# Optimization experiments

Hardware: AMD Instinct MI355X
Metric: run time of the kernel (lower is better)

The kernel has to match this reference:

```python
import jax, jax.numpy as jnp
import numpy as np

M = 4096
N = 4096

def _twiddle(L):
    k = jnp.arange(L, dtype=jnp.float32)
    ang = -np.pi * k / (2.0 * L)
    return jnp.stack([jnp.cos(ang), jnp.sin(ang)], axis=-1).astype(jnp.float32)  # [L,2] = exp(-i*pi*k/(2L))

def setup_inputs() -> dict:
    key = jax.random.key(0)
    x = jax.random.normal(key, (M, N), dtype=jnp.float32)
    return {"x": x, "expkM": _twiddle(M), "expkN": _twiddle(N)}

def reference(x, expkM, expkN):
    # 2D DCT-II via Makhoul even/odd reordering + single complex FFT2 + twiddle multiply.
    # out[u,v] = sum_{m,n} x[m,n] cos(pi*u*(2m+1)/(2M)) cos(pi*v*(2n+1)/(2N))
    Mh, Nh = x.shape
    permM = jnp.concatenate([jnp.arange(0, Mh, 2), jnp.arange(Mh - 1, 0, -2)])
    permN = jnp.concatenate([jnp.arange(0, Nh, 2), jnp.arange(Nh - 1, 0, -2)])
    y = x[permM][:, permN]                       # even/odd reorder in both dims
    Y = jnp.fft.fft2(y)                          # [M,N] complex
    wM = expkM[:, 0] + 1j * expkM[:, 1]          # exp(-i*pi*u/(2M))
    wN = expkN[:, 0] + 1j * expkN[:, 1]          # exp(-i*pi*v/(2N))
    Yrev = jnp.roll(Y[::-1, :], 1, axis=0)       # Y[(M-u) % M, v]
    C = 0.5 * (wN[None, :] * Y + jnp.conj(wN)[None, :] * jnp.conj(Yrev))
    return jnp.real(wM[:, None] * C)
```

## Files before the change

kernel.cpp:

```cpp
#include <hip/hip_runtime.h>
#include <math.h>

#define NFULL 4096
#define NH    2048
#define T     256

__device__ __forceinline__ int pad(int i) { return i + (i >> 3); }

__device__ __forceinline__ float2 cmul(float2 a, float2 b) {
    return make_float2(a.x * b.x - a.y * b.y, a.x * b.y + a.y * b.x);
}

__device__ __forceinline__ float2 sc(float ang) {
    float s, c;
    __sincosf(ang, &s, &c);
    return make_float2(c, s);
}

__device__ __forceinline__ void dft8(float2 v[8]) {
    const float s = 0.70710678118654752f;
    float2 e0 = v[0], o0 = v[1], e1 = v[2], o1 = v[3];
    float2 e2 = v[4], o2 = v[5], e3 = v[6], o3 = v[7];
    float2 t0 = make_float2(e0.x + e2.x, e0.y + e2.y);
    float2 t1 = make_float2(e0.x - e2.x, e0.y - e2.y);
    float2 t2 = make_float2(e1.x + e3.x, e1.y + e3.y);
    float2 t3 = make_float2(e1.x - e3.x, e1.y - e3.y);
    float2 E0 = make_float2(t0.x + t2.x, t0.y + t2.y);
    float2 E2 = make_float2(t0.x - t2.x, t0.y - t2.y);
    float2 E1 = make_float2(t1.x + t3.y, t1.y - t3.x);
    float2 E3 = make_float2(t1.x - t3.y, t1.y + t3.x);
    float2 u0 = make_float2(o0.x + o2.x, o0.y + o2.y);
    float2 u1 = make_float2(o0.x - o2.x, o0.y - o2.y);
    float2 u2 = make_float2(o1.x + o3.x, o1.y + o3.y);
    float2 u3 = make_float2(o1.x - o3.x, o1.y - o3.y);
    float2 O0 = make_float2(u0.x + u2.x, u0.y + u2.y);
    float2 O2 = make_float2(u0.x - u2.x, u0.y - u2.y);
    float2 O1 = make_float2(u1.x + u3.y, u1.y - u3.x);
    float2 O3 = make_float2(u1.x - u3.y, u1.y + u3.x);
    O1 = make_float2(s * (O1.x + O1.y), s * (O1.y - O1.x));
    O2 = make_float2(O2.y, -O2.x);
    O3 = make_float2(s * (O3.y - O3.x), s * (-O3.x - O3.y));
    v[0] = make_float2(E0.x + O0.x, E0.y + O0.y);
    v[4] = make_float2(E0.x - O0.x, E0.y - O0.y);
    v[1] = make_float2(E1.x + O1.x, E1.y + O1.y);
    v[5] = make_float2(E1.x - O1.x, E1.y - O1.y);
    v[2] = make_float2(E2.x + O2.x, E2.y + O2.y);
    v[6] = make_float2(E2.x - O2.x, E2.y - O2.y);
    v[3] = make_float2(E3.x + O3.x, E3.y + O3.y);
    v[7] = make_float2(E3.x - O3.x, E3.y - O3.y);
}

__device__ __forceinline__ void dft4(float2 v[4]) {
    float2 t0 = make_float2(v[0].x + v[2].x, v[0].y + v[2].y);
    float2 t1 = make_float2(v[0].x - v[2].x, v[0].y - v[2].y);
    float2 t2 = make_float2(v[1].x + v[3].x, v[1].y + v[3].y);
    float2 t3 = make_float2(v[1].x - v[3].x, v[1].y - v[3].y);
    v[0] = make_float2(t0.x + t2.x, t0.y + t2.y);
    v[2] = make_float2(t0.x - t2.x, t0.y - t2.y);
    v[1] = make_float2(t1.x + t3.y, t1.y - t3.x);
    v[3] = make_float2(t1.x - t3.y, t1.y + t3.x);
}

__global__ __launch_bounds__(T) void dct_rows_rfft(const float* __restrict__ in,
                                                   const float* __restrict__ expk,
                                                   float* __restrict__ out) {
    __shared__ float2 A[NH + (NH >> 3)];
    __shared__ float2 B[NH + (NH >> 3)];
    const int row = blockIdx.x;
    const int t = threadIdx.x;
    const float4* __restrict__ src4 = (const float4*)(in + (size_t)row * NFULL);

    float4 f0 = src4[t], f1 = src4[t + T], f2 = src4[t + 2 * T], f3 = src4[t + 3 * T];

    A[pad(t)]                  = make_float2(f0.x, f0.z);
    A[pad(2047 - t)]           = make_float2(f0.w, f0.y);
    A[pad(t + T)]              = make_float2(f1.x, f1.z);
    A[pad(2047 - (t + T))]     = make_float2(f1.w, f1.y);
    A[pad(t + 2 * T)]          = make_float2(f2.x, f2.z);
    A[pad(2047 - (t + 2 * T))] = make_float2(f2.w, f2.y);
    A[pad(t + 3 * T)]          = make_float2(f3.x, f3.z);
    A[pad(2047 - (t + 3 * T))] = make_float2(f3.w, f3.y);
    __syncthreads();

    float2 v[8];
    {
        #pragma unroll
        for (int r = 0; r < 8; ++r) v[r] = A[pad(t + 256 * r)];
        dft8(v);
        #pragma unroll
        for (int r = 0; r < 8; ++r) B[pad(8 * t + r)] = v[r];
    }
    __syncthreads();
    {
        #pragma unroll
        for (int r = 0; r < 8; ++r) v[r] = B[pad(t + 256 * r)];
        const float a = -(float)M_PI / 32.0f * (float)(t & 7);
        float2 w1 = sc(a), w2 = sc(2.0f * a), w4 = sc(4.0f * a);
        float2 w3 = cmul(w1, w2), w5 = cmul(w1, w4), w6 = cmul(w2, w4);
        float2 w7 = cmul(w3, w4);
        v[1] = cmul(v[1], w1); v[2] = cmul(v[2], w2); v[3] = cmul(v[3], w3);
        v[4] = cmul(v[4], w4); v[5] = cmul(v[5], w5); v[6] = cmul(v[6], w6);
        v[7] = cmul(v[7], w7);
        dft8(v);
        const int d = ((t >> 3) << 6) + (t & 7);
        #pragma unroll
        for (int r = 0; r < 8; ++r) A[pad(d + 8 * r)] = v[r];
    }
    __syncthreads();
    {
        #pragma unroll
        for (int r = 0; r < 8; ++r) v[r] = A[pad(t + 256 * r)];
        const float a = -(float)M_PI / 256.0f * (float)(t & 63);
        float2 w1 = sc(a), w2 = sc(2.0f * a), w4 = sc(4.0f * a);
        float2 w3 = cmul(w1, w2), w5 = cmul(w1, w4), w6 = cmul(w2, w4);
        float2 w7 = cmul(w3, w4);
        v[1] = cmul(v[1], w1); v[2] = cmul(v[2], w2); v[3] = cmul(v[3], w3);
        v[4] = cmul(v[4], w4); v[5] = cmul(v[5], w5); v[6] = cmul(v[6], w6);
        v[7] = cmul(v[7], w7);
        dft8(v);
        const int d = ((t >> 6) << 9) + (t & 63);
        #pragma unroll
        for (int r = 0; r < 8; ++r) B[pad(d + 64 * r)] = v[r];
    }
    __syncthreads();
    #pragma unroll
    for (int h = 0; h < 2; ++h) {
        const int j = t + 256 * h;
        float2 u[4];
        #pragma unroll
        for (int r = 0; r < 4; ++r) u[r] = B[pad(j + 512 * r)];
        const float a = -(float)M_PI / 1024.0f * (float)j;
        float2 w1 = sc(a), w2 = sc(2.0f * a);
        float2 w3 = cmul(w1, w2);
        u[1] = cmul(u[1], w1);
        u[2] = cmul(u[2], w2);
        u[3] = cmul(u[3], w3);
        dft4(u);
        #pragma unroll
        for (int r = 0; r < 4; ++r) A[pad(j + 512 * r)] = u[r];
    }
    __syncthreads();

    const float2* __restrict__ ek = (const float2*)expk;
    float* __restrict__ dst = out + (size_t)row * NFULL;
    #pragma unroll
    for (int i = 0; i < 8; ++i) {
        const int k = t + T * i;
        if (k == 0) {
            float2 z0 = A[pad(0)];
            dst[0]  = ek[0].x * (z0.x + z0.y);
            dst[NH] = ek[NH].x * (z0.x - z0.y);
        } else {
            float2 Zk = A[pad(k)];
            float2 Zr = A[pad(NH - k)];
            float2 E = make_float2(0.5f * (Zk.x + Zr.x), 0.5f * (Zk.y - Zr.y));
            float2 O = make_float2(0.5f * (Zk.y + Zr.y), 0.5f * (Zr.x - Zk.x));
            float2 uu = sc(-(float)M_PI / 2048.0f * (float)k);
            float2 Y = make_float2(E.x + uu.x * O.x - uu.y * O.y,
                                   E.y + uu.x * O.y + uu.y * O.x);
            float2 wk = ek[k];
            dst[k] = wk.x * Y.x - wk.y * Y.y;
            float2 wn = ek[NFULL - k];
            dst[NFULL - k] = wn.x * Y.x + wn.y * Y.y;
        }
    }
}

__global__ __launch_bounds__(256) void transpose4k(const float* __restrict__ in,
                                                   float* __restrict__ out) {
    __shared__ float tile[32][33];
    const int x0 = blockIdx.x * 32;
    const int y0 = blockIdx.y * 32;
    const int tx = threadIdx.x & 31;
    const int ty = threadIdx.x >> 5;

    #pragma unroll
    for (int i = 0; i < 32; i += 8)
        tile[ty + i][tx] = in[(size_t)(y0 + ty + i) * NFULL + (x0 + tx)];
    __syncthreads();
    #pragma unroll
    for (int i = 0; i < 32; i += 8)
        out[(size_t)(x0 + ty + i) * NFULL + (y0 + tx)] = tile[tx][ty + i];
}

extern "C" void kernel_launch(void* const* d_in, const int* in_sizes, int n_in,
                              void* d_out, int out_size, void* d_ws, size_t ws_size,
                              hipStream_t stream) {
    const float* x     = (const float*)d_in[0];
    const float* expkM = (const float*)d_in[1];
    const float* expkN = (const float*)d_in[2];
    float* out = (float*)d_out;
    float* ws1 = (float*)d_ws;

    dct_rows_rfft<<<NFULL, T, 0, stream>>>(x, expkN, ws1);
    transpose4k<<<dim3(128, 128), 256, 0, stream>>>(ws1, out);
    dct_rows_rfft<<<NFULL, T, 0, stream>>>(out, expkM, ws1);
    transpose4k<<<dim3(128, 128), 256, 0, stream>>>(ws1, out);
}
```

Before: 104.1 us.

## Load FFT inputs directly into registers and swizzle shared memory instead of padding

Each thread now reads its first-stage radix-8 inputs straight from global memory, including the mirrored odd samples, so the initial shared-memory staging pass and one barrier go away. Shared-memory indexing switches from padding to an XOR swizzle, which shrinks the two buffers, and launch bounds now ask for 5 blocks per SM to raise occupancy. The reversed float4 loads are less sequential per wavefront, and the swizzle may leave some bank conflicts in certain stages.

```diff
diff --git a/kernel.cpp b/kernel.cpp
--- a/kernel.cpp
+++ b/kernel.cpp
@@ -5,7 +5,7 @@
 #define NH    2048
 #define T     256
 
-__device__ __forceinline__ int pad(int i) { return i + (i >> 3); }
+__device__ __forceinline__ int sw(int i) { return i ^ (((i >> 4) & 7) << 1); }
 
 __device__ __forceinline__ float2 cmul(float2 a, float2 b) {
     return make_float2(a.x * b.x - a.y * b.y, a.x * b.y + a.y * b.x);
@@ -61,39 +61,41 @@
     v[3] = make_float2(t1.x - t3.y, t1.y + t3.x);
 }
 
-__global__ __launch_bounds__(T) void dct_rows_rfft(const float* __restrict__ in,
-                                                   const float* __restrict__ expk,
-                                                   float* __restrict__ out) {
-    __shared__ float2 A[NH + (NH >> 3)];
-    __shared__ float2 B[NH + (NH >> 3)];
+__global__ __launch_bounds__(T, 5) void dct_rows_rfft(const float* __restrict__ in,
+                                                      const float* __restrict__ expk,
+                                                      float* __restrict__ out) {
+    __shared__ float2 A[NH];
+    __shared__ float2 B[NH];
     const int row = blockIdx.x;
     const int t = threadIdx.x;
     const float4* __restrict__ src4 = (const float4*)(in + (size_t)row * NFULL);
 
-    float4 f0 = src4[t], f1 = src4[t + T], f2 = src4[t + 2 * T], f3 = src4[t + 3 * T];
-
-    A[pad(t)]                  = make_float2(f0.x, f0.z);
-    A[pad(2047 - t)]           = make_float2(f0.w, f0.y);
-    A[pad(t + T)]              = make_float2(f1.x, f1.z);
-    A[pad(2047 - (t + T))]     = make_float2(f1.w, f1.y);
-    A[pad(t + 2 * T)]          = make_float2(f2.x, f2.z);
-    A[pad(2047 - (t + 2 * T))] = make_float2(f2.w, f2.y);
-    A[pad(t + 3 * T)]          = make_float2(f3.x, f3.z);
-    A[pad(2047 - (t + 3 * T))] = make_float2(f3.w, f3.y);
-    __syncthreads();
-
     float2 v[8];
     {
-        #pragma unroll
-        for (int r = 0; r < 8; ++r) v[r] = A[pad(t + 256 * r)];
+        float4 f0 = src4[t];
+        float4 f1 = src4[t + 256];
+        float4 f2 = src4[t + 512];
+        float4 f3 = src4[t + 768];
+        float4 g3 = src4[1023 - t];
+        float4 g2 = src4[767 - t];
+        float4 g1 = src4[511 - t];
+        float4 g0 = src4[255 - t];
+        v[0] = make_float2(f0.x, f0.z);
+        v[1] = make_float2(f1.x, f1.z);
+        v[2] = make_float2(f2.x, f2.z);
+        v[3] = make_float2(f3.x, f3.z);
+        v[4] = make_float2(g3.w, g3.y);
+        v[5] = make_float2(g2.w, g2.y);
+        v[6] = make_float2(g1.w, g1.y);
+        v[7] = make_float2(g0.w, g0.y);
         dft8(v);
         #pragma unroll
-        for (int r = 0; r < 8; ++r) B[pad(8 * t + r)] = v[r];
+        for (int r = 0; r < 8; ++r) B[sw(8 * t + r)] = v[r];
     }
     __syncthreads();
     {
         #pragma unroll
-        for (int r = 0; r < 8; ++r) v[r] = B[pad(t + 256 * r)];
+        for (int r = 0; r < 8; ++r) v[r] = B[sw(t + 256 * r)];
         const float a = -(float)M_PI / 32.0f * (float)(t & 7);
         float2 w1 = sc(a), w2 = sc(2.0f * a), w4 = sc(4.0f * a);
         float2 w3 = cmul(w1, w2), w5 = cmul(w1, w4), w6 = cmul(w2, w4);
@@ -104,12 +106,12 @@
         dft8(v);
         const int d = ((t >> 3) << 6) + (t & 7);
         #pragma unroll
-        for (int r = 0; r < 8; ++r) A[pad(d + 8 * r)] = v[r];
+        for (int r = 0; r < 8; ++r) A[sw(d + 8 * r)] = v[r];
     }
     __syncthreads();
     {
         #pragma unroll
-        for (int r = 0; r < 8; ++r) v[r] = A[pad(t + 256 * r)];
+        for (int r = 0; r < 8; ++r) v[r] = A[sw(t + 256 * r)];
         const float a = -(float)M_PI / 256.0f * (float)(t & 63);
         float2 w1 = sc(a), w2 = sc(2.0f * a), w4 = sc(4.0f * a);
         float2 w3 = cmul(w1, w2), w5 = cmul(w1, w4), w6 = cmul(w2, w4);
@@ -120,7 +122,7 @@
         dft8(v);
         const int d = ((t >> 6) << 9) + (t & 63);
         #pragma unroll
-        for (int r = 0; r < 8; ++r) B[pad(d + 64 * r)] = v[r];
+        for (int r = 0; r < 8; ++r) B[sw(d + 64 * r)] = v[r];
     }
     __syncthreads();
     #pragma unroll
@@ -128,7 +130,7 @@
         const int j = t + 256 * h;
         float2 u[4];
         #pragma unroll
-        for (int r = 0; r < 4; ++r) u[r] = B[pad(j + 512 * r)];
+        for (int r = 0; r < 4; ++r) u[r] = B[sw(j + 512 * r)];
         const float a = -(float)M_PI / 1024.0f * (float)j;
         float2 w1 = sc(a), w2 = sc(2.0f * a);
         float2 w3 = cmul(w1, w2);
@@ -137,7 +139,7 @@
         u[3] = cmul(u[3], w3);
         dft4(u);
         #pragma unroll
-        for (int r = 0; r < 4; ++r) A[pad(j + 512 * r)] = u[r];
+        for (int r = 0; r < 4; ++r) A[sw(j + 512 * r)] = u[r];
     }
     __syncthreads();
 
@@ -147,12 +149,12 @@
     for (int i = 0; i < 8; ++i) {
         const int k = t + T * i;
         if (k == 0) {
-            float2 z0 = A[pad(0)];
+            float2 z0 = A[sw(0)];
             dst[0]  = ek[0].x * (z0.x + z0.y);
             dst[NH] = ek[NH].x * (z0.x - z0.y);
         } else {
-            float2 Zk = A[pad(k)];
-            float2 Zr = A[pad(NH - k)];
+            float2 Zk = A[sw(k)];
+            float2 Zr = A[sw(NH - k)];
             float2 E = make_float2(0.5f * (Zk.x + Zr.x), 0.5f * (Zk.y - Zr.y));
             float2 O = make_float2(0.5f * (Zk.y + Zr.y), 0.5f * (Zr.x - Zk.x));
             float2 uu = sc(-(float)M_PI / 2048.0f * (float)k);
```

Result: slower. 113.5 us (+9.1%).
